# Optimization experiments

Measured on AMD Instinct MI355X. Metric: run time of the kernel, lower is better.

Reference implementation:

```python
import jax, jax.numpy as jnp
import numpy as np

EPS = 1e-6

def layernorm2d(x, w, b):
    # x: [B,C,H,W]; normalize over channel dim per spatial location
    mu = jnp.mean(x, axis=1, keepdims=True)
    var = jnp.var(x, axis=1, keepdims=True)
    xn = (x - mu) / jnp.sqrt(var + EPS)
    return xn * w[None, :, None, None] + b[None, :, None, None]

def mish(x):
    return x * jnp.tanh(jax.nn.softplus(x))

def setup_inputs() -> dict:
    key = jax.random.key(0)
    ks = jax.random.split(key, 16)
    B, C, H, W, T = 16, 192, 96, 96, 512
    s = 0.02
    return {
        "t": jax.random.normal(ks[0], (B, T), jnp.float32),
        "x_l": jax.random.normal(ks[1], (B, C, H, W), jnp.float32),
        "x_r": jax.random.normal(ks[2], (B, C, H, W), jnp.float32),
        "ln_wl": jnp.ones((C,), jnp.float32),
        "ln_bl": jnp.zeros((C,), jnp.float32),
        "ln_wr": jnp.ones((C,), jnp.float32),
        "ln_br": jnp.zeros((C,), jnp.float32),
        "Wl1": jax.random.normal(ks[3], (C, C), jnp.float32) * s,
        "bl1": jnp.zeros((C,), jnp.float32),
        "Wr1": jax.random.normal(ks[4], (C, C), jnp.float32) * s,
        "br1": jnp.zeros((C,), jnp.float32),
        "Wl2": jax.random.normal(ks[5], (C, C), jnp.float32) * s,
        "bl2": jnp.zeros((C,), jnp.float32),
        "Wr2": jax.random.normal(ks[6], (C, C), jnp.float32) * s,
        "br2": jnp.zeros((C,), jnp.float32),
        "beta": jnp.zeros((C,), jnp.float32),
        "gamma": jnp.zeros((C,), jnp.float32),
        "Wt": jax.random.normal(ks[7], (C, T), jnp.float32) * s,
        "bt": jnp.zeros((C,), jnp.float32),
    }

def reference(t, x_l, x_r, ln_wl, ln_bl, ln_wr, ln_br,
              Wl1, bl1, Wr1, br1, Wl2, bl2, Wr2, br2,
              beta, gamma, Wt, bt):
    C = x_l.shape[1]
    scale = C ** (-0.5)
    # 1x1 convs as channel einsums; outputs in bhwc layout
    Q_l = jnp.einsum('bchw,oc->bhwo', layernorm2d(x_l, ln_wl, ln_bl), Wl1) + bl1  # [B,H,Wl,C]
    Q_r = jnp.einsum('bchw,oc->bhwo', layernorm2d(x_r, ln_wr, ln_br), Wr1) + br1  # [B,H,Wr,C]
    V_l = jnp.einsum('bchw,oc->bhwo', x_l, Wl2) + bl2
    V_r = jnp.einsum('bchw,oc->bhwo', x_r, Wr2) + br2
    att = jnp.einsum('bhxc,bhyc->bhxy', Q_l, Q_r) * scale  # [B,H,Wl,Wr]
    F_r2l = jnp.einsum('bhxy,bhyc->bhxc', jax.nn.softmax(att, axis=-1), V_r)
    F_l2r = jnp.einsum('bhxy,bhxc->bhyc', jax.nn.softmax(att, axis=2), V_l)
    temb = (mish(t) @ Wt.T + bt)[:, :, None, None]  # [B,C,1,1]
    out_l = x_l + jnp.transpose(F_r2l, (0, 3, 1, 2)) * beta[None, :, None, None] + temb
    out_r = x_r + jnp.transpose(F_l2r, (0, 3, 1, 2)) * gamma[None, :, None, None] + temb
    return (out_l, out_r)
```

## Files before the change

kernel.cpp:

```cpp
#include <hip/hip_runtime.h>
#include <hip/hip_bf16.h>


typedef __attribute__((ext_vector_type(8))) short bhalf8;
typedef __attribute__((ext_vector_type(4))) float f32x4;

#define DEVI static __device__ __forceinline__

constexpr int Cc   = 192;
constexpr int HWc  = 9216;
constexpr int CHW  = 192 * 9216;
constexpr int HALF_OUT = 16 * CHW;
constexpr int PS   = 104;
constexpr int AS   = 100;

DEVI unsigned short f2bf(float f) {
  __hip_bfloat16 h = __float2bfloat16(f);
  return __builtin_bit_cast(unsigned short, h);
}
DEVI unsigned pk2bf(float a, float b) {
  return (unsigned)f2bf(a) | ((unsigned)f2bf(b) << 16);
}
DEVI float bf2f(unsigned short h) {
  unsigned u = (unsigned)h << 16;
  return __builtin_bit_cast(float, u);
}
DEVI float bf2f_s(short h) { return bf2f((unsigned short)h); }

__global__ void setup1(
    const float* __restrict__ t,
    const float* __restrict__ lnwl, const float* __restrict__ lnbl,
    const float* __restrict__ lnwr, const float* __restrict__ lnbr,
    const float* __restrict__ Wl1, const float* __restrict__ bl1,
    const float* __restrict__ Wr1, const float* __restrict__ br1,
    const float* __restrict__ Wl2, const float* __restrict__ Wr2,
    short* __restrict__ W1l_b, short* __restrict__ W1r_b,
    short* __restrict__ W2l_b, short* __restrict__ W2r_b,
    float* __restrict__ s1l, float* __restrict__ t1l,
    float* __restrict__ s1r, float* __restrict__ t1r,
    float* __restrict__ mt)
{
  const int blk = blockIdx.x, tid = threadIdx.x;
  if (blk < 576) {
    int id  = blk * 256 + tid;
    int m   = id / 36864;
    int rem = id - m * 36864;
    int c   = rem % 192;
    float v;
    short* dst;
    if (m == 0)      { v = lnwl[c] * Wl1[rem]; dst = W1l_b; }
    else if (m == 1) { v = lnwr[c] * Wr1[rem]; dst = W1r_b; }
    else if (m == 2) { v = Wl2[rem];           dst = W2l_b; }
    else             { v = Wr2[rem];           dst = W2r_b; }
    dst[rem] = (short)f2bf(v);
  } else if (blk == 576 || blk == 577) {
    if (tid < 192) {
      const float* Wm = (blk == 576) ? Wl1 : Wr1;
      const float* lw = (blk == 576) ? lnwl : lnwr;
      const float* lb = (blk == 576) ? lnbl : lnbr;
      const float* bb = (blk == 576) ? bl1 : br1;
      float s = 0.f, tb = 0.f;
      for (int c = 0; c < 192; ++c) {
        float wv = Wm[tid * 192 + c];
        s  += lw[c] * wv;
        tb += lb[c] * wv;
      }
      if (blk == 576) { s1l[tid] = s; t1l[tid] = tb + bb[tid]; }
      else            { s1r[tid] = s; t1r[tid] = tb + bb[tid]; }
    }
  } else {
    int id = (blk - 578) * 256 + tid;
    float v = t[id];
    float sp = (v > 20.f) ? v : log1pf(__expf(v));
    mt[id] = v * tanhf(sp);
  }
}

__global__ void setup2(const float* __restrict__ mt, const float* __restrict__ Wt,
                       const float* __restrict__ bt, float* __restrict__ temb)
{
  int id = blockIdx.x * 256 + threadIdx.x;
  int b = id / 192, o = id - b * 192;
  float s = 0.f;
  for (int k = 0; k < 512; ++k) s += mt[b * 512 + k] * Wt[o * 512 + k];
  temb[id] = s + bt[o];
}

struct SmemT {
  short buf1[96 * 200];
  short buf2[19968];
  short vtl[192 * PS];
  short vtr[192 * PS];
  float misc[960];
};
static_assert(sizeof(SmemT) <= 163840, "LDS overflow");

__launch_bounds__(768, 3)
__global__ void scam_main(
    const float* __restrict__ x_l, const float* __restrict__ x_r,
    const float* __restrict__ bl2, const float* __restrict__ br2,
    const float* __restrict__ beta, const float* __restrict__ gamma,
    const short* __restrict__ W1l_b, const short* __restrict__ W1r_b,
    const short* __restrict__ W2l_b, const short* __restrict__ W2r_b,
    const float* __restrict__ s1l, const float* __restrict__ t1l,
    const float* __restrict__ s1r, const float* __restrict__ t1r,
    const float* __restrict__ temb,
    float* __restrict__ out)
{
  __shared__ SmemT sm;
  const int tid  = threadIdx.x;
  const int lane = tid & 63;
  const int wid  = tid >> 6;
  const int m16  = lane & 15;
  const int hb   = lane >> 4;
  const int kc8  = hb * 8;
  const int r4   = hb * 4;
  const int slice = blockIdx.x;
  const int bb_ = slice / 96;
  const int hh_ = slice - bb_ * 96;
  const int sliceBase = bb_ * CHW + hh_ * 96;
  const int o_wm = wid * 16 + m16;

  if (tid < 576) {
    int a = tid / 192, o = tid - a * 192;
    if (a == 0)      sm.misc[384 + o] = temb[bb_ * 192 + o];
    else if (a == 1) sm.misc[576 + o] = beta[o];
    else             sm.misc[768 + o] = gamma[o];
  }

  #pragma unroll
  for (int j = 0; j < 6; ++j) {
    int i4 = j * 768 + tid;
    int c  = i4 / 24;
    int w4 = i4 - c * 24;
    const float4 xl4 = *reinterpret_cast<const float4*>(x_l + sliceBase + c * HWc + w4 * 4);
    const float4 xr4 = *reinterpret_cast<const float4*>(x_r + sliceBase + c * HWc + w4 * 4);
    int sw = ((((c >> 3) ^ (w4 & 7)) << 3) | (c & 7));
    int base = w4 * 800 + sw;
    sm.buf1[base      ] = (short)f2bf(xl4.x);
    sm.buf1[base + 200] = (short)f2bf(xl4.y);
    sm.buf1[base + 400] = (short)f2bf(xl4.z);
    sm.buf1[base + 600] = (short)f2bf(xl4.w);
    sm.buf2[base      ] = (short)f2bf(xr4.x);
    sm.buf2[base + 200] = (short)f2bf(xr4.y);
    sm.buf2[base + 400] = (short)f2bf(xr4.z);
    sm.buf2[base + 600] = (short)f2bf(xr4.w);
  }
  __syncthreads();

  {
    int side = (tid >= 384) ? 1 : 0;
    int rest = tid - side * 384;
    int w = rest >> 2;
    int q = rest & 3;
    const short* Xb = side ? sm.buf2 : sm.buf1;
    const int kxw = (w >> 2) & 7;
    float s0 = 0.f, s2 = 0.f;
    #pragma unroll
    for (int mc = 0; mc < 6; ++mc) {
      bhalf8 v = *reinterpret_cast<const bhalf8*>(Xb + w * 200 + (((q * 6 + mc) ^ kxw) << 3));
      #pragma unroll
      for (int e = 0; e < 8; ++e) { float f = bf2f_s(v[e]); s0 += f; s2 += f * f; }
    }
    s0 += __shfl_xor(s0, 1); s2 += __shfl_xor(s2, 1);
    s0 += __shfl_xor(s0, 2); s2 += __shfl_xor(s2, 2);
    if (q == 0) {
      float mu  = s0 * (1.f / 192.f);
      float var = s2 * (1.f / 192.f) - mu * mu;
      float rs  = rsqrtf(var + 1e-6f);
      sm.misc[side * 192 + w]      = mu;
      sm.misc[side * 192 + 96 + w] = rs;
    }
  }

  #pragma unroll
  for (int sd = 0; sd < 2; ++sd) {
    const short* Wb = sd ? W2r_b : W2l_b;
    const short* Xb = sd ? sm.buf2 : sm.buf1;
    short* Vt = sd ? sm.vtr : sm.vtl;
    const float bv = (sd ? br2 : bl2)[o_wm];
    bhalf8 af[6];
    #pragma unroll
    for (int k = 0; k < 6; ++k)
      af[k] = *reinterpret_cast<const bhalf8*>(Wb + o_wm * 192 + k * 32 + kc8);
    #pragma unroll
    for (int xi = 0; xi < 6; ++xi) {
      const int row = xi * 16 + m16;
      const int kxr = (row >> 2) & 7;
      const short* Xr = Xb + row * 200;
      f32x4 acc = {0.f, 0.f, 0.f, 0.f};
      #pragma unroll
      for (int k = 0; k < 6; ++k) {
        bhalf8 bfr = *reinterpret_cast<const bhalf8*>(Xr + (((k * 4 + hb) ^ kxr) << 3));
        acc = __builtin_amdgcn_mfma_f32_16x16x32_bf16(bfr, af[k], acc, 0, 0, 0);
      }
      uint2 pv;
      pv.x = pk2bf(acc[0] + bv, acc[1] + bv);
      pv.y = pk2bf(acc[2] + bv, acc[3] + bv);
      *reinterpret_cast<uint2*>(Vt + o_wm * PS + xi * 16 + r4) = pv;
    }
  }

  f32x4 accQ0[6], accQ1[6];
  {
    {
      bhalf8 bfq[6];
      #pragma unroll
      for (int k = 0; k < 6; ++k)
        bfq[k] = *reinterpret_cast<const bhalf8*>(W1l_b + o_wm * 192 + k * 32 + kc8);
      #pragma unroll
      for (int mi = 0; mi < 6; ++mi) {
        const int row = mi * 16 + m16;
        const int kxr = (row >> 2) & 7;
        const short* Xr = sm.buf1 + row * 200;
        f32x4 acc = {0.f, 0.f, 0.f, 0.f};
        #pragma unroll
        for (int k = 0; k < 6; ++k) {
          bhalf8 afr = *reinterpret_cast<const bhalf8*>(Xr + (((k * 4 + hb) ^ kxr) << 3));
          acc = __builtin_amdgcn_mfma_f32_16x16x32_bf16(bfq[k], afr, acc, 0, 0, 0);
        }
        accQ0[mi] = acc;
      }
    }
    {
      bhalf8 bfq[6];
      #pragma unroll
      for (int k = 0; k < 6; ++k)
        bfq[k] = *reinterpret_cast<const bhalf8*>(W1r_b + o_wm * 192 + k * 32 + kc8);
      #pragma unroll
      for (int mi = 0; mi < 6; ++mi) {
        const int row = mi * 16 + m16;
        const int kxr = (row >> 2) & 7;
        const short* Xr = sm.buf2 + row * 200;
        f32x4 acc = {0.f, 0.f, 0.f, 0.f};
        #pragma unroll
        for (int k = 0; k < 6; ++k) {
          bhalf8 afr = *reinterpret_cast<const bhalf8*>(Xr + (((k * 4 + hb) ^ kxr) << 3));
          acc = __builtin_amdgcn_mfma_f32_16x16x32_bf16(bfq[k], afr, acc, 0, 0, 0);
        }
        accQ1[mi] = acc;
      }
    }
  }
  __syncthreads();
  {
    const int obase = wid * 16 + r4;
    const int oblk  = obase >> 3;
    const int osub  = (hb & 1) * 4;
    #pragma unroll
    for (int sd = 0; sd < 2; ++sd) {
      short* Qb = sd ? sm.buf2 : sm.buf1;
      const float* muA = sm.misc + sd * 192;
      const float* rsA = muA + 96;
      const float* s1g = sd ? s1r : s1l;
      const float* t1g = sd ? t1r : t1l;
      float s1v[4], t1v[4];
      #pragma unroll
      for (int j = 0; j < 4; ++j) { s1v[j] = s1g[obase + j]; t1v[j] = t1g[obase + j]; }
      #pragma unroll
      for (int mi = 0; mi < 6; ++mi) {
        const int x = mi * 16 + m16;
        const int kx = (x >> 2) & 7;
        float mu = muA[x], rs = rsA[x];
        float mrs = mu * rs;
        f32x4 acc = sd ? accQ1[mi] : accQ0[mi];
        float q0 = rs * acc[0] - mrs * s1v[0] + t1v[0];
        float q1 = rs * acc[1] - mrs * s1v[1] + t1v[1];
        float q2 = rs * acc[2] - mrs * s1v[2] + t1v[2];
        float q3 = rs * acc[3] - mrs * s1v[3] + t1v[3];
        uint2 pv;
        pv.x = pk2bf(q0, q1);
        pv.y = pk2bf(q2, q3);
        *reinterpret_cast<uint2*>(Qb + x * 200 + (((oblk ^ kx) << 3) | osub)) = pv;
      }
    }
  }
  __syncthreads();

  {
    const int mi = wid >> 1;
    const int yb = (wid & 1) * 3;
    const int arow = mi * 16 + m16;
    const int kxa = (arow >> 2) & 7;
    bhalf8 afa[6];
    #pragma unroll
    for (int k = 0; k < 6; ++k)
      afa[k] = *reinterpret_cast<const bhalf8*>(sm.buf1 + arow * 200 + (((k * 4 + hb) ^ kxa) << 3));
    f32x4 accA[3];
    #pragma unroll
    for (int yt = 0; yt < 3; ++yt) {
      const int brow = (yb + yt) * 16 + m16;
      const int kxb = (brow >> 2) & 7;
      const short* Br = sm.buf2 + brow * 200;
      f32x4 acc = {0.f, 0.f, 0.f, 0.f};
      #pragma unroll
      for (int k = 0; k < 6; ++k) {
        bhalf8 bfy = *reinterpret_cast<const bhalf8*>(Br + (((k * 4 + hb) ^ kxb) << 3));
        acc = __builtin_amdgcn_mfma_f32_16x16x32_bf16(afa[k], bfy, acc, 0, 0, 0);
      }
      accA[yt] = acc;
    }
    __syncthreads();
    float* attf = reinterpret_cast<float*>(sm.buf1);
    const float scale = 0.07216878364870323f;
    #pragma unroll
    for (int yt = 0; yt < 3; ++yt) {
      #pragma unroll
      for (int j = 0; j < 4; ++j) {
        int x = mi * 16 + r4 + j;
        int y = (yb + yt) * 16 + m16;
        attf[x * AS + (y ^ (x & 31))] = accA[yt][j] * scale;
      }
    }
  }
  __syncthreads();

  {
    const float* attf = reinterpret_cast<const float*>(sm.buf1);
    short* Pr = sm.buf2;
    short* Pc = sm.buf2 + 96 * PS;
    const int r = tid >> 3;
    const int p = tid & 7;
    {
      float av[12];
      #pragma unroll
      for (int k = 0; k < 12; ++k)
        av[k] = attf[r * AS + ((p * 12 + k) ^ (r & 31))];
      float mx = av[0];
      #pragma unroll
      for (int k = 1; k < 12; ++k) mx = fmaxf(mx, av[k]);
      mx = fmaxf(mx, __shfl_xor(mx, 1));
      mx = fmaxf(mx, __shfl_xor(mx, 2));
      mx = fmaxf(mx, __shfl_xor(mx, 4));
      float s = 0.f;
      #pragma unroll
      for (int k = 0; k < 12; ++k) { av[k] = __expf(av[k] - mx); s += av[k]; }
      s += __shfl_xor(s, 1); s += __shfl_xor(s, 2); s += __shfl_xor(s, 4);
      float inv = 1.f / s;
      #pragma unroll
      for (int k = 0; k < 12; k += 2) {
        *reinterpret_cast<unsigned*>(Pr + r * PS + p * 12 + k) =
            pk2bf(av[k] * inv, av[k + 1] * inv);
      }
    }
    {
      float av[12];
      #pragma unroll
      for (int k = 0; k < 12; ++k) {
        int x = p * 12 + k;
        av[k] = attf[x * AS + (r ^ (x & 31))];
      }
      float mx = av[0];
      #pragma unroll
      for (int k = 1; k < 12; ++k) mx = fmaxf(mx, av[k]);
      mx = fmaxf(mx, __shfl_xor(mx, 1));
      mx = fmaxf(mx, __shfl_xor(mx, 2));
      mx = fmaxf(mx, __shfl_xor(mx, 4));
      float s = 0.f;
      #pragma unroll
      for (int k = 0; k < 12; ++k) { av[k] = __expf(av[k] - mx); s += av[k]; }
      s += __shfl_xor(s, 1); s += __shfl_xor(s, 2); s += __shfl_xor(s, 4);
      float inv = 1.f / s;
      #pragma unroll
      for (int k = 0; k < 12; k += 2) {
        *reinterpret_cast<unsigned*>(Pc + r * PS + p * 12 + k) =
            pk2bf(av[k] * inv, av[k + 1] * inv);
      }
    }
  }
  __syncthreads();

  f32x4 accF[6], accG[6];
  {
    const short* Pr = sm.buf2;
    const short* Pc = sm.buf2 + 96 * PS;
    bhalf8 vf[3], vg[3];
    #pragma unroll
    for (int k = 0; k < 3; ++k) {
      vf[k] = *reinterpret_cast<const bhalf8*>(sm.vtr + o_wm * PS + k * 32 + kc8);
      vg[k] = *reinterpret_cast<const bhalf8*>(sm.vtl + o_wm * PS + k * 32 + kc8);
    }
    #pragma unroll
    for (int xi = 0; xi < 6; ++xi) {
      f32x4 a1 = {0.f, 0.f, 0.f, 0.f}, a2 = {0.f, 0.f, 0.f, 0.f};
      #pragma unroll
      for (int k = 0; k < 3; ++k) {
        bhalf8 ap = *reinterpret_cast<const bhalf8*>(Pr + (xi * 16 + m16) * PS + k * 32 + kc8);
        a1 = __builtin_amdgcn_mfma_f32_16x16x32_bf16(vf[k], ap, a1, 0, 0, 0);
        bhalf8 aq = *reinterpret_cast<const bhalf8*>(Pc + (xi * 16 + m16) * PS + k * 32 + kc8);
        a2 = __builtin_amdgcn_mfma_f32_16x16x32_bf16(vg[k], aq, a2, 0, 0, 0);
      }
      accF[xi] = a1; accG[xi] = a2;
    }
  }
  __syncthreads();
  {
    const int cblk = (wid * 16 + r4) >> 3;
    const int csub = (hb & 1) * 4;
    #pragma unroll
    for (int xi = 0; xi < 6; ++xi) {
      const int x = xi * 16 + m16;
      const int kx = (x >> 2) & 7;
      const int off = x * 200 + (((cblk ^ kx) << 3) | csub);
      uint2 pf, pg;
      pf.x = pk2bf(accF[xi][0], accF[xi][1]);
      pf.y = pk2bf(accF[xi][2], accF[xi][3]);
      pg.x = pk2bf(accG[xi][0], accG[xi][1]);
      pg.y = pk2bf(accG[xi][2], accG[xi][3]);
      *reinterpret_cast<uint2*>(sm.buf1 + off) = pf;
      *reinterpret_cast<uint2*>(sm.buf2 + off) = pg;
    }
  }
  __syncthreads();

  #pragma unroll
  for (int sd = 0; sd < 2; ++sd) {
    const float* xg = sd ? x_r : x_l;
    float* og = out + (sd ? HALF_OUT : 0);
    const short* Fb = sd ? sm.buf2 : sm.buf1;
    const float* coef = sm.misc + (sd ? 768 : 576);
    #pragma unroll
    for (int j = 0; j < 6; ++j) {
      int i4 = j * 768 + tid;
      int c  = i4 / 24;
      int w4 = i4 - c * 24;
      const float4 xv = *reinterpret_cast<const float4*>(xg + sliceBase + c * HWc + w4 * 4);
      float cf = coef[c];
      float tv = sm.misc[384 + c];
      int sw = ((((c >> 3) ^ (w4 & 7)) << 3) | (c & 7));
      int fb = w4 * 800 + sw;
      float4 ov;
      ov.x = xv.x + bf2f_s(Fb[fb      ]) * cf + tv;
      ov.y = xv.y + bf2f_s(Fb[fb + 200]) * cf + tv;
      ov.z = xv.z + bf2f_s(Fb[fb + 400]) * cf + tv;
      ov.w = xv.w + bf2f_s(Fb[fb + 600]) * cf + tv;
      *reinterpret_cast<float4*>(og + sliceBase + c * HWc + w4 * 4) = ov;
    }
  }
}

extern "C" void kernel_launch(void* const* d_in, const int* in_sizes, int n_in,
                              void* d_out, int out_size, void* d_ws, size_t ws_size,
                              hipStream_t stream)
{
  const float* t    = (const float*)d_in[0];
  const float* x_l  = (const float*)d_in[1];
  const float* x_r  = (const float*)d_in[2];
  const float* lnwl = (const float*)d_in[3];
  const float* lnbl = (const float*)d_in[4];
  const float* lnwr = (const float*)d_in[5];
  const float* lnbr = (const float*)d_in[6];
  const float* Wl1  = (const float*)d_in[7];
  const float* bl1  = (const float*)d_in[8];
  const float* Wr1  = (const float*)d_in[9];
  const float* br1  = (const float*)d_in[10];
  const float* Wl2  = (const float*)d_in[11];
  const float* bl2  = (const float*)d_in[12];
  const float* Wr2  = (const float*)d_in[13];
  const float* br2  = (const float*)d_in[14];
  const float* beta = (const float*)d_in[15];
  const float* gamma= (const float*)d_in[16];
  const float* Wt   = (const float*)d_in[17];
  const float* bt   = (const float*)d_in[18];
  float* out = (float*)d_out;

  char* ws = (char*)d_ws;
  short* W1l_b = (short*)ws;
  short* W1r_b = W1l_b + 36864;
  short* W2l_b = W1r_b + 36864;
  short* W2r_b = W2l_b + 36864;
  float* fws  = (float*)(ws + 4 * 73728);
  float* s1l  = fws;
  float* t1l  = fws + 192;
  float* s1r  = fws + 384;
  float* t1r  = fws + 576;
  float* temb = fws + 768;
  float* mt   = fws + 3840;

  setup1<<<610, 256, 0, stream>>>(t, lnwl, lnbl, lnwr, lnbr, Wl1, bl1, Wr1, br1,
                                  Wl2, Wr2, W1l_b, W1r_b, W2l_b, W2r_b,
                                  s1l, t1l, s1r, t1r, mt);
  setup2<<<12, 256, 0, stream>>>(mt, Wt, bt, temb);
  scam_main<<<1536, 768, 0, stream>>>(x_l, x_r, bl2, br2, beta, gamma,
                                      W1l_b, W1r_b, W2l_b, W2r_b,
                                      s1l, t1l, s1r, t1r, temb, out);
}
```

Before: 262.7 us.

## Use 1024-thread blocks with extra waves for memory phases only

Blocks grow from 768 to 1024 threads. The four extra waves help only with the global load/store phases, and all MFMA stages are gated to the first 12 waves. The input load phase now issues all global float4 loads into registers before the bf16 conversion and LDS stores, and the epilogue likewise batches x_l and x_r loads ahead of the output writes, aiming for more memory-level parallelism. In exchange the min-blocks hint of 3 is dropped and register arrays grow, which may lower occupancy and leave idle waves during compute phases.

```diff
diff --git a/kernel.cpp b/kernel.cpp
--- a/kernel.cpp
+++ b/kernel.cpp
@@ -95,7 +95,7 @@
 };
 static_assert(sizeof(SmemT) <= 163840, "LDS overflow");
 
-__launch_bounds__(768, 3)
+__launch_bounds__(1024)
 __global__ void scam_main(
     const float* __restrict__ x_l, const float* __restrict__ x_r,
     const float* __restrict__ bl2, const float* __restrict__ br2,
@@ -128,27 +128,40 @@
     else             sm.misc[768 + o] = gamma[o];
   }
 
-  #pragma unroll
-  for (int j = 0; j < 6; ++j) {
-    int i4 = j * 768 + tid;
-    int c  = i4 / 24;
-    int w4 = i4 - c * 24;
-    const float4 xl4 = *reinterpret_cast<const float4*>(x_l + sliceBase + c * HWc + w4 * 4);
-    const float4 xr4 = *reinterpret_cast<const float4*>(x_r + sliceBase + c * HWc + w4 * 4);
-    int sw = ((((c >> 3) ^ (w4 & 7)) << 3) | (c & 7));
-    int base = w4 * 800 + sw;
-    sm.buf1[base      ] = (short)f2bf(xl4.x);
-    sm.buf1[base + 200] = (short)f2bf(xl4.y);
-    sm.buf1[base + 400] = (short)f2bf(xl4.z);
-    sm.buf1[base + 600] = (short)f2bf(xl4.w);
-    sm.buf2[base      ] = (short)f2bf(xr4.x);
-    sm.buf2[base + 200] = (short)f2bf(xr4.y);
-    sm.buf2[base + 400] = (short)f2bf(xr4.z);
-    sm.buf2[base + 600] = (short)f2bf(xr4.w);
-  }
-  __syncthreads();
-
   {
+    float4 xl4[5], xr4[5];
+    #pragma unroll
+    for (int j = 0; j < 5; ++j) {
+      int i4 = j * 1024 + tid;
+      if (i4 < 4608) {
+        int c  = i4 / 24;
+        int w4 = i4 - c * 24;
+        xl4[j] = *reinterpret_cast<const float4*>(x_l + sliceBase + c * HWc + w4 * 4);
+        xr4[j] = *reinterpret_cast<const float4*>(x_r + sliceBase + c * HWc + w4 * 4);
+      }
+    }
+    #pragma unroll
+    for (int j = 0; j < 5; ++j) {
+      int i4 = j * 1024 + tid;
+      if (i4 < 4608) {
+        int c  = i4 / 24;
+        int w4 = i4 - c * 24;
+        int sw = ((((c >> 3) ^ (w4 & 7)) << 3) | (c & 7));
+        int base = w4 * 800 + sw;
+        sm.buf1[base      ] = (short)f2bf(xl4[j].x);
+        sm.buf1[base + 200] = (short)f2bf(xl4[j].y);
+        sm.buf1[base + 400] = (short)f2bf(xl4[j].z);
+        sm.buf1[base + 600] = (short)f2bf(xl4[j].w);
+        sm.buf2[base      ] = (short)f2bf(xr4[j].x);
+        sm.buf2[base + 200] = (short)f2bf(xr4[j].y);
+        sm.buf2[base + 400] = (short)f2bf(xr4[j].z);
+        sm.buf2[base + 600] = (short)f2bf(xr4[j].w);
+      }
+    }
+  }
+  __syncthreads();
+
+  if (tid < 768) {
     int side = (tid >= 384) ? 1 : 0;
     int rest = tid - side * 384;
     int w = rest >> 2;
@@ -173,36 +186,38 @@
     }
   }
 
-  #pragma unroll
-  for (int sd = 0; sd < 2; ++sd) {
-    const short* Wb = sd ? W2r_b : W2l_b;
-    const short* Xb = sd ? sm.buf2 : sm.buf1;
-    short* Vt = sd ? sm.vtr : sm.vtl;
-    const float bv = (sd ? br2 : bl2)[o_wm];
-    bhalf8 af[6];
-    #pragma unroll
-    for (int k = 0; k < 6; ++k)
-      af[k] = *reinterpret_cast<const bhalf8*>(Wb + o_wm * 192 + k * 32 + kc8);
-    #pragma unroll
-    for (int xi = 0; xi < 6; ++xi) {
-      const int row = xi * 16 + m16;
-      const int kxr = (row >> 2) & 7;
-      const short* Xr = Xb + row * 200;
-      f32x4 acc = {0.f, 0.f, 0.f, 0.f};
-      #pragma unroll
-      for (int k = 0; k < 6; ++k) {
-        bhalf8 bfr = *reinterpret_cast<const bhalf8*>(Xr + (((k * 4 + hb) ^ kxr) << 3));
-        acc = __builtin_amdgcn_mfma_f32_16x16x32_bf16(bfr, af[k], acc, 0, 0, 0);
-      }
-      uint2 pv;
-      pv.x = pk2bf(acc[0] + bv, acc[1] + bv);
-      pv.y = pk2bf(acc[2] + bv, acc[3] + bv);
-      *reinterpret_cast<uint2*>(Vt + o_wm * PS + xi * 16 + r4) = pv;
+  if (wid < 12) {
+    #pragma unroll
+    for (int sd = 0; sd < 2; ++sd) {
+      const short* Wb = sd ? W2r_b : W2l_b;
+      const short* Xb = sd ? sm.buf2 : sm.buf1;
+      short* Vt = sd ? sm.vtr : sm.vtl;
+      const float bv = (sd ? br2 : bl2)[o_wm];
+      bhalf8 af[6];
+      #pragma unroll
+      for (int k = 0; k < 6; ++k)
+        af[k] = *reinterpret_cast<const bhalf8*>(Wb + o_wm * 192 + k * 32 + kc8);
+      #pragma unroll
+      for (int xi = 0; xi < 6; ++xi) {
+        const int row = xi * 16 + m16;
+        const int kxr = (row >> 2) & 7;
+        const short* Xr = Xb + row * 200;
+        f32x4 acc = {0.f, 0.f, 0.f, 0.f};
+        #pragma unroll
+        for (int k = 0; k < 6; ++k) {
+          bhalf8 bfr = *reinterpret_cast<const bhalf8*>(Xr + (((k * 4 + hb) ^ kxr) << 3));
+          acc = __builtin_amdgcn_mfma_f32_16x16x32_bf16(bfr, af[k], acc, 0, 0, 0);
+        }
+        uint2 pv;
+        pv.x = pk2bf(acc[0] + bv, acc[1] + bv);
+        pv.y = pk2bf(acc[2] + bv, acc[3] + bv);
+        *reinterpret_cast<uint2*>(Vt + o_wm * PS + xi * 16 + r4) = pv;
+      }
     }
   }
 
   f32x4 accQ0[6], accQ1[6];
-  {
+  if (wid < 12) {
     {
       bhalf8 bfq[6];
       #pragma unroll
@@ -243,7 +258,7 @@
     }
   }
   __syncthreads();
-  {
+  if (wid < 12) {
     const int obase = wid * 16 + r4;
     const int oblk  = obase >> 3;
     const int osub  = (hb & 1) * 4;
@@ -278,44 +293,48 @@
   __syncthreads();
 
   {
+    f32x4 accA[3];
     const int mi = wid >> 1;
     const int yb = (wid & 1) * 3;
-    const int arow = mi * 16 + m16;
-    const int kxa = (arow >> 2) & 7;
-    bhalf8 afa[6];
-    #pragma unroll
-    for (int k = 0; k < 6; ++k)
-      afa[k] = *reinterpret_cast<const bhalf8*>(sm.buf1 + arow * 200 + (((k * 4 + hb) ^ kxa) << 3));
-    f32x4 accA[3];
-    #pragma unroll
-    for (int yt = 0; yt < 3; ++yt) {
-      const int brow = (yb + yt) * 16 + m16;
-      const int kxb = (brow >> 2) & 7;
-      const short* Br = sm.buf2 + brow * 200;
-      f32x4 acc = {0.f, 0.f, 0.f, 0.f};
-      #pragma unroll
-      for (int k = 0; k < 6; ++k) {
-        bhalf8 bfy = *reinterpret_cast<const bhalf8*>(Br + (((k * 4 + hb) ^ kxb) << 3));
-        acc = __builtin_amdgcn_mfma_f32_16x16x32_bf16(afa[k], bfy, acc, 0, 0, 0);
-      }
-      accA[yt] = acc;
+    if (wid < 12) {
+      const int arow = mi * 16 + m16;
+      const int kxa = (arow >> 2) & 7;
+      bhalf8 afa[6];
+      #pragma unroll
+      for (int k = 0; k < 6; ++k)
+        afa[k] = *reinterpret_cast<const bhalf8*>(sm.buf1 + arow * 200 + (((k * 4 + hb) ^ kxa) << 3));
+      #pragma unroll
+      for (int yt = 0; yt < 3; ++yt) {
+        const int brow = (yb + yt) * 16 + m16;
+        const int kxb = (brow >> 2) & 7;
+        const short* Br = sm.buf2 + brow * 200;
+        f32x4 acc = {0.f, 0.f, 0.f, 0.f};
+        #pragma unroll
+        for (int k = 0; k < 6; ++k) {
+          bhalf8 bfy = *reinterpret_cast<const bhalf8*>(Br + (((k * 4 + hb) ^ kxb) << 3));
+          acc = __builtin_amdgcn_mfma_f32_16x16x32_bf16(afa[k], bfy, acc, 0, 0, 0);
+        }
+        accA[yt] = acc;
+      }
     }
     __syncthreads();
-    float* attf = reinterpret_cast<float*>(sm.buf1);
-    const float scale = 0.07216878364870323f;
-    #pragma unroll
-    for (int yt = 0; yt < 3; ++yt) {
-      #pragma unroll
-      for (int j = 0; j < 4; ++j) {
-        int x = mi * 16 + r4 + j;
-        int y = (yb + yt) * 16 + m16;
-        attf[x * AS + (y ^ (x & 31))] = accA[yt][j] * scale;
-      }
-    }
-  }
-  __syncthreads();
-
-  {
+    if (wid < 12) {
+      float* attf = reinterpret_cast<float*>(sm.buf1);
+      const float scale = 0.07216878364870323f;
+      #pragma unroll
+      for (int yt = 0; yt < 3; ++yt) {
+        #pragma unroll
+        for (int j = 0; j < 4; ++j) {
+          int x = mi * 16 + r4 + j;
+          int y = (yb + yt) * 16 + m16;
+          attf[x * AS + (y ^ (x & 31))] = accA[yt][j] * scale;
+        }
+      }
+    }
+  }
+  __syncthreads();
+
+  if (tid < 768) {
     const float* attf = reinterpret_cast<const float*>(sm.buf1);
     short* Pr = sm.buf2;
     short* Pc = sm.buf2 + 96 * PS;
@@ -371,7 +390,7 @@
   __syncthreads();
 
   f32x4 accF[6], accG[6];
-  {
+  if (wid < 12) {
     const short* Pr = sm.buf2;
     const short* Pc = sm.buf2 + 96 * PS;
     bhalf8 vf[3], vg[3];
@@ -394,7 +413,7 @@
     }
   }
   __syncthreads();
-  {
+  if (wid < 12) {
     const int cblk = (wid * 16 + r4) >> 3;
     const int csub = (hb & 1) * 4;
     #pragma unroll
@@ -413,28 +432,42 @@
   }
   __syncthreads();
 
-  #pragma unroll
-  for (int sd = 0; sd < 2; ++sd) {
-    const float* xg = sd ? x_r : x_l;
-    float* og = out + (sd ? HALF_OUT : 0);
-    const short* Fb = sd ? sm.buf2 : sm.buf1;
-    const float* coef = sm.misc + (sd ? 768 : 576);
-    #pragma unroll
-    for (int j = 0; j < 6; ++j) {
-      int i4 = j * 768 + tid;
-      int c  = i4 / 24;
-      int w4 = i4 - c * 24;
-      const float4 xv = *reinterpret_cast<const float4*>(xg + sliceBase + c * HWc + w4 * 4);
-      float cf = coef[c];
-      float tv = sm.misc[384 + c];
-      int sw = ((((c >> 3) ^ (w4 & 7)) << 3) | (c & 7));
-      int fb = w4 * 800 + sw;
-      float4 ov;
-      ov.x = xv.x + bf2f_s(Fb[fb      ]) * cf + tv;
-      ov.y = xv.y + bf2f_s(Fb[fb + 200]) * cf + tv;
-      ov.z = xv.z + bf2f_s(Fb[fb + 400]) * cf + tv;
-      ov.w = xv.w + bf2f_s(Fb[fb + 600]) * cf + tv;
-      *reinterpret_cast<float4*>(og + sliceBase + c * HWc + w4 * 4) = ov;
+  {
+    float4 xvl[5], xvr[5];
+    #pragma unroll
+    for (int j = 0; j < 5; ++j) {
+      int i4 = j * 1024 + tid;
+      if (i4 < 4608) {
+        int c  = i4 / 24;
+        int w4 = i4 - c * 24;
+        xvl[j] = *reinterpret_cast<const float4*>(x_l + sliceBase + c * HWc + w4 * 4);
+        xvr[j] = *reinterpret_cast<const float4*>(x_r + sliceBase + c * HWc + w4 * 4);
+      }
+    }
+    #pragma unroll
+    for (int sd = 0; sd < 2; ++sd) {
+      float* og = out + (sd ? HALF_OUT : 0);
+      const short* Fb = sd ? sm.buf2 : sm.buf1;
+      const float* coef = sm.misc + (sd ? 768 : 576);
+      #pragma unroll
+      for (int j = 0; j < 5; ++j) {
+        int i4 = j * 1024 + tid;
+        if (i4 < 4608) {
+          int c  = i4 / 24;
+          int w4 = i4 - c * 24;
+          const float4 xv = sd ? xvr[j] : xvl[j];
+          float cf = coef[c];
+          float tv = sm.misc[384 + c];
+          int sw = ((((c >> 3) ^ (w4 & 7)) << 3) | (c & 7));
+          int fb = w4 * 800 + sw;
+          float4 ov;
+          ov.x = xv.x + bf2f_s(Fb[fb      ]) * cf + tv;
+          ov.y = xv.y + bf2f_s(Fb[fb + 200]) * cf + tv;
+          ov.z = xv.z + bf2f_s(Fb[fb + 400]) * cf + tv;
+          ov.w = xv.w + bf2f_s(Fb[fb + 600]) * cf + tv;
+          *reinterpret_cast<float4*>(og + sliceBase + c * HWc + w4 * 4) = ov;
+        }
+      }
     }
   }
 }
@@ -481,7 +514,7 @@
                                   Wl2, Wr2, W1l_b, W1r_b, W2l_b, W2r_b,
                                   s1l, t1l, s1r, t1r, mt);
   setup2<<<12, 256, 0, stream>>>(mt, Wt, bt, temb);
-  scam_main<<<1536, 768, 0, stream>>>(x_l, x_r, bl2, br2, beta, gamma,
-                                      W1l_b, W1r_b, W2l_b, W2r_b,
-                                      s1l, t1l, s1r, t1r, temb, out);
-}
+  scam_main<<<1536, 1024, 0, stream>>>(x_l, x_r, bl2, br2, beta, gamma,
+                                       W1l_b, W1r_b, W2l_b, W2r_b,
+                                       s1l, t1l, s1r, t1r, temb, out);
+}
```

Result: slower. 269.5 us (+2.6%).

## Keep V projections in registers and halve LDS to fit two workgroups per CU

Applied to the files above, without the earlier changes.

The V projection outputs now stay in registers as MFMA-layout fragments instead of being written to transposed LDS buffers. They feed 16x16x16 bf16 MFMAs directly against the softmax matrices. The Q projections for left and right are processed one after the other with an extra barrier, so only one accumulator set is live. LDS shrinks to under 80 KB and launch bounds move to 6 waves-per-EU so two 768-thread workgroups can share a CU. The cost is more barriers, the narrower K=16 MFMA, and higher register pressure from holding the V fragments across phases.

```diff
diff --git a/kernel.cpp b/kernel.cpp
--- a/kernel.cpp
+++ b/kernel.cpp
@@ -3,6 +3,7 @@
 
 
 typedef __attribute__((ext_vector_type(8))) short bhalf8;
+typedef __attribute__((ext_vector_type(4))) short bhalf4;
 typedef __attribute__((ext_vector_type(4))) float f32x4;
 
 #define DEVI static __device__ __forceinline__
@@ -11,7 +12,7 @@
 constexpr int HWc  = 9216;
 constexpr int CHW  = 192 * 9216;
 constexpr int HALF_OUT = 16 * CHW;
-constexpr int PS   = 104;
+constexpr int PPS  = 100;
 constexpr int AS   = 100;
 
 DEVI unsigned short f2bf(float f) {
@@ -87,15 +88,13 @@
 }
 
 struct SmemT {
-  short buf1[96 * 200];
-  short buf2[19968];
-  short vtl[192 * PS];
-  short vtr[192 * PS];
+  short buf1[19200];
+  short buf2[19200];
   float misc[960];
 };
-static_assert(sizeof(SmemT) <= 163840, "LDS overflow");
-
-__launch_bounds__(768, 3)
+static_assert(sizeof(SmemT) <= 81920, "LDS overflow for 2 WGs/CU");
+
+__launch_bounds__(768, 6)
 __global__ void scam_main(
     const float* __restrict__ x_l, const float* __restrict__ x_r,
     const float* __restrict__ bl2, const float* __restrict__ br2,
@@ -173,11 +172,11 @@
     }
   }
 
+  uint2 vRl[6], vRr[6];
   #pragma unroll
   for (int sd = 0; sd < 2; ++sd) {
     const short* Wb = sd ? W2r_b : W2l_b;
     const short* Xb = sd ? sm.buf2 : sm.buf1;
-    short* Vt = sd ? sm.vtr : sm.vtl;
     const float bv = (sd ? br2 : bl2)[o_wm];
     bhalf8 af[6];
     #pragma unroll
@@ -197,49 +196,28 @@
       uint2 pv;
       pv.x = pk2bf(acc[0] + bv, acc[1] + bv);
       pv.y = pk2bf(acc[2] + bv, acc[3] + bv);
-      *reinterpret_cast<uint2*>(Vt + o_wm * PS + xi * 16 + r4) = pv;
-    }
-  }
-
-  f32x4 accQ0[6], accQ1[6];
-  {
-    {
-      bhalf8 bfq[6];
-      #pragma unroll
-      for (int k = 0; k < 6; ++k)
-        bfq[k] = *reinterpret_cast<const bhalf8*>(W1l_b + o_wm * 192 + k * 32 + kc8);
-      #pragma unroll
-      for (int mi = 0; mi < 6; ++mi) {
-        const int row = mi * 16 + m16;
-        const int kxr = (row >> 2) & 7;
-        const short* Xr = sm.buf1 + row * 200;
-        f32x4 acc = {0.f, 0.f, 0.f, 0.f};
-        #pragma unroll
-        for (int k = 0; k < 6; ++k) {
-          bhalf8 afr = *reinterpret_cast<const bhalf8*>(Xr + (((k * 4 + hb) ^ kxr) << 3));
-          acc = __builtin_amdgcn_mfma_f32_16x16x32_bf16(bfq[k], afr, acc, 0, 0, 0);
-        }
-        accQ0[mi] = acc;
-      }
-    }
-    {
-      bhalf8 bfq[6];
-      #pragma unroll
-      for (int k = 0; k < 6; ++k)
-        bfq[k] = *reinterpret_cast<const bhalf8*>(W1r_b + o_wm * 192 + k * 32 + kc8);
-      #pragma unroll
-      for (int mi = 0; mi < 6; ++mi) {
-        const int row = mi * 16 + m16;
-        const int kxr = (row >> 2) & 7;
-        const short* Xr = sm.buf2 + row * 200;
-        f32x4 acc = {0.f, 0.f, 0.f, 0.f};
-        #pragma unroll
-        for (int k = 0; k < 6; ++k) {
-          bhalf8 afr = *reinterpret_cast<const bhalf8*>(Xr + (((k * 4 + hb) ^ kxr) << 3));
-          acc = __builtin_amdgcn_mfma_f32_16x16x32_bf16(bfq[k], afr, acc, 0, 0, 0);
-        }
-        accQ1[mi] = acc;
-      }
+      if (sd) vRr[xi] = pv; else vRl[xi] = pv;
+    }
+  }
+
+  f32x4 accQ[6];
+  {
+    bhalf8 bfq[6];
+    #pragma unroll
+    for (int k = 0; k < 6; ++k)
+      bfq[k] = *reinterpret_cast<const bhalf8*>(W1l_b + o_wm * 192 + k * 32 + kc8);
+    #pragma unroll
+    for (int mi = 0; mi < 6; ++mi) {
+      const int row = mi * 16 + m16;
+      const int kxr = (row >> 2) & 7;
+      const short* Xr = sm.buf1 + row * 200;
+      f32x4 acc = {0.f, 0.f, 0.f, 0.f};
+      #pragma unroll
+      for (int k = 0; k < 6; ++k) {
+        bhalf8 afr = *reinterpret_cast<const bhalf8*>(Xr + (((k * 4 + hb) ^ kxr) << 3));
+        acc = __builtin_amdgcn_mfma_f32_16x16x32_bf16(bfq[k], afr, acc, 0, 0, 0);
+      }
+      accQ[mi] = acc;
     }
   }
   __syncthreads();
@@ -247,32 +225,68 @@
     const int obase = wid * 16 + r4;
     const int oblk  = obase >> 3;
     const int osub  = (hb & 1) * 4;
-    #pragma unroll
-    for (int sd = 0; sd < 2; ++sd) {
-      short* Qb = sd ? sm.buf2 : sm.buf1;
-      const float* muA = sm.misc + sd * 192;
-      const float* rsA = muA + 96;
-      const float* s1g = sd ? s1r : s1l;
-      const float* t1g = sd ? t1r : t1l;
-      float s1v[4], t1v[4];
-      #pragma unroll
-      for (int j = 0; j < 4; ++j) { s1v[j] = s1g[obase + j]; t1v[j] = t1g[obase + j]; }
-      #pragma unroll
-      for (int mi = 0; mi < 6; ++mi) {
-        const int x = mi * 16 + m16;
-        const int kx = (x >> 2) & 7;
-        float mu = muA[x], rs = rsA[x];
-        float mrs = mu * rs;
-        f32x4 acc = sd ? accQ1[mi] : accQ0[mi];
-        float q0 = rs * acc[0] - mrs * s1v[0] + t1v[0];
-        float q1 = rs * acc[1] - mrs * s1v[1] + t1v[1];
-        float q2 = rs * acc[2] - mrs * s1v[2] + t1v[2];
-        float q3 = rs * acc[3] - mrs * s1v[3] + t1v[3];
-        uint2 pv;
-        pv.x = pk2bf(q0, q1);
-        pv.y = pk2bf(q2, q3);
-        *reinterpret_cast<uint2*>(Qb + x * 200 + (((oblk ^ kx) << 3) | osub)) = pv;
-      }
+    const float* muA = sm.misc;
+    const float* rsA = sm.misc + 96;
+    float s1v[4], t1v[4];
+    #pragma unroll
+    for (int j = 0; j < 4; ++j) { s1v[j] = s1l[obase + j]; t1v[j] = t1l[obase + j]; }
+    #pragma unroll
+    for (int mi = 0; mi < 6; ++mi) {
+      const int x = mi * 16 + m16;
+      const int kx = (x >> 2) & 7;
+      float mu = muA[x], rs = rsA[x];
+      float mrs = mu * rs;
+      f32x4 acc = accQ[mi];
+      uint2 pv;
+      pv.x = pk2bf(rs * acc[0] - mrs * s1v[0] + t1v[0],
+                   rs * acc[1] - mrs * s1v[1] + t1v[1]);
+      pv.y = pk2bf(rs * acc[2] - mrs * s1v[2] + t1v[2],
+                   rs * acc[3] - mrs * s1v[3] + t1v[3]);
+      *reinterpret_cast<uint2*>(sm.buf1 + x * 200 + (((oblk ^ kx) << 3) | osub)) = pv;
+    }
+  }
+  {
+    bhalf8 bfq[6];
+    #pragma unroll
+    for (int k = 0; k < 6; ++k)
+      bfq[k] = *reinterpret_cast<const bhalf8*>(W1r_b + o_wm * 192 + k * 32 + kc8);
+    #pragma unroll
+    for (int mi = 0; mi < 6; ++mi) {
+      const int row = mi * 16 + m16;
+      const int kxr = (row >> 2) & 7;
+      const short* Xr = sm.buf2 + row * 200;
+      f32x4 acc = {0.f, 0.f, 0.f, 0.f};
+      #pragma unroll
+      for (int k = 0; k < 6; ++k) {
+        bhalf8 afr = *reinterpret_cast<const bhalf8*>(Xr + (((k * 4 + hb) ^ kxr) << 3));
+        acc = __builtin_amdgcn_mfma_f32_16x16x32_bf16(bfq[k], afr, acc, 0, 0, 0);
+      }
+      accQ[mi] = acc;
+    }
+  }
+  __syncthreads();
+  {
+    const int obase = wid * 16 + r4;
+    const int oblk  = obase >> 3;
+    const int osub  = (hb & 1) * 4;
+    const float* muA = sm.misc + 192;
+    const float* rsA = sm.misc + 288;
+    float s1v[4], t1v[4];
+    #pragma unroll
+    for (int j = 0; j < 4; ++j) { s1v[j] = s1r[obase + j]; t1v[j] = t1r[obase + j]; }
+    #pragma unroll
+    for (int mi = 0; mi < 6; ++mi) {
+      const int x = mi * 16 + m16;
+      const int kx = (x >> 2) & 7;
+      float mu = muA[x], rs = rsA[x];
+      float mrs = mu * rs;
+      f32x4 acc = accQ[mi];
+      uint2 pv;
+      pv.x = pk2bf(rs * acc[0] - mrs * s1v[0] + t1v[0],
+                   rs * acc[1] - mrs * s1v[1] + t1v[1]);
+      pv.y = pk2bf(rs * acc[2] - mrs * s1v[2] + t1v[2],
+                   rs * acc[3] - mrs * s1v[3] + t1v[3]);
+      *reinterpret_cast<uint2*>(sm.buf2 + x * 200 + (((oblk ^ kx) << 3) | osub)) = pv;
     }
   }
   __syncthreads();
@@ -318,7 +332,7 @@
   {
     const float* attf = reinterpret_cast<const float*>(sm.buf1);
     short* Pr = sm.buf2;
-    short* Pc = sm.buf2 + 96 * PS;
+    short* Pc = sm.buf2 + 96 * PPS;
     const int r = tid >> 3;
     const int p = tid & 7;
     {
@@ -339,7 +353,7 @@
       float inv = 1.f / s;
       #pragma unroll
       for (int k = 0; k < 12; k += 2) {
-        *reinterpret_cast<unsigned*>(Pr + r * PS + p * 12 + k) =
+        *reinterpret_cast<unsigned*>(Pr + r * PPS + p * 12 + k) =
             pk2bf(av[k] * inv, av[k + 1] * inv);
       }
     }
@@ -363,51 +377,61 @@
       float inv = 1.f / s;
       #pragma unroll
       for (int k = 0; k < 12; k += 2) {
-        *reinterpret_cast<unsigned*>(Pc + r * PS + p * 12 + k) =
+        *reinterpret_cast<unsigned*>(Pc + r * PPS + p * 12 + k) =
             pk2bf(av[k] * inv, av[k + 1] * inv);
       }
     }
   }
   __syncthreads();
 
-  f32x4 accF[6], accG[6];
+  f32x4 accL[6];
   {
     const short* Pr = sm.buf2;
-    const short* Pc = sm.buf2 + 96 * PS;
-    bhalf8 vf[3], vg[3];
-    #pragma unroll
-    for (int k = 0; k < 3; ++k) {
-      vf[k] = *reinterpret_cast<const bhalf8*>(sm.vtr + o_wm * PS + k * 32 + kc8);
-      vg[k] = *reinterpret_cast<const bhalf8*>(sm.vtl + o_wm * PS + k * 32 + kc8);
-    }
-    #pragma unroll
-    for (int xi = 0; xi < 6; ++xi) {
-      f32x4 a1 = {0.f, 0.f, 0.f, 0.f}, a2 = {0.f, 0.f, 0.f, 0.f};
-      #pragma unroll
-      for (int k = 0; k < 3; ++k) {
-        bhalf8 ap = *reinterpret_cast<const bhalf8*>(Pr + (xi * 16 + m16) * PS + k * 32 + kc8);
-        a1 = __builtin_amdgcn_mfma_f32_16x16x32_bf16(vf[k], ap, a1, 0, 0, 0);
-        bhalf8 aq = *reinterpret_cast<const bhalf8*>(Pc + (xi * 16 + m16) * PS + k * 32 + kc8);
-        a2 = __builtin_amdgcn_mfma_f32_16x16x32_bf16(vg[k], aq, a2, 0, 0, 0);
-      }
-      accF[xi] = a1; accG[xi] = a2;
-    }
-  }
-  __syncthreads();
-  {
+    const short* Pc = sm.buf2 + 96 * PPS;
     const int cblk = (wid * 16 + r4) >> 3;
     const int csub = (hb & 1) * 4;
     #pragma unroll
-    for (int xi = 0; xi < 6; ++xi) {
-      const int x = xi * 16 + m16;
+    for (int xt = 0; xt < 6; ++xt) {
+      const int x = xt * 16 + m16;
+      f32x4 acc = {0.f, 0.f, 0.f, 0.f};
+      #pragma unroll
+      for (int kt = 0; kt < 6; ++kt) {
+        bhalf4 a = __builtin_bit_cast(bhalf4, vRr[kt]);
+        bhalf4 b = *reinterpret_cast<const bhalf4*>(Pr + x * PPS + kt * 16 + hb * 4);
+        acc = __builtin_amdgcn_mfma_f32_16x16x16bf16_1k(a, b, acc, 0, 0, 0);
+      }
       const int kx = (x >> 2) & 7;
       const int off = x * 200 + (((cblk ^ kx) << 3) | csub);
-      uint2 pf, pg;
-      pf.x = pk2bf(accF[xi][0], accF[xi][1]);
-      pf.y = pk2bf(accF[xi][2], accF[xi][3]);
-      pg.x = pk2bf(accG[xi][0], accG[xi][1]);
-      pg.y = pk2bf(accG[xi][2], accG[xi][3]);
+      uint2 pf;
+      pf.x = pk2bf(acc[0], acc[1]);
+      pf.y = pk2bf(acc[2], acc[3]);
       *reinterpret_cast<uint2*>(sm.buf1 + off) = pf;
+    }
+    #pragma unroll
+    for (int yt = 0; yt < 6; ++yt) {
+      const int y = yt * 16 + m16;
+      f32x4 acc = {0.f, 0.f, 0.f, 0.f};
+      #pragma unroll
+      for (int kt = 0; kt < 6; ++kt) {
+        bhalf4 a = __builtin_bit_cast(bhalf4, vRl[kt]);
+        bhalf4 b = *reinterpret_cast<const bhalf4*>(Pc + y * PPS + kt * 16 + hb * 4);
+        acc = __builtin_amdgcn_mfma_f32_16x16x16bf16_1k(a, b, acc, 0, 0, 0);
+      }
+      accL[yt] = acc;
+    }
+  }
+  __syncthreads();
+  {
+    const int cblk = (wid * 16 + r4) >> 3;
+    const int csub = (hb & 1) * 4;
+    #pragma unroll
+    for (int yt = 0; yt < 6; ++yt) {
+      const int y = yt * 16 + m16;
+      const int kx = (y >> 2) & 7;
+      const int off = y * 200 + (((cblk ^ kx) << 3) | csub);
+      uint2 pg;
+      pg.x = pk2bf(accL[yt][0], accL[yt][1]);
+      pg.y = pk2bf(accL[yt][2], accL[yt][3]);
       *reinterpret_cast<uint2*>(sm.buf2 + off) = pg;
     }
   }
```

Result: slower. 622.0 us (+136.8%).
